# Kernel tuning notes

Measured on AMD Instinct MI355X. Metric: run time of the kernel, lower is better.

Reference implementation:

```python
import jax, jax.numpy as jnp
import numpy as np

EPS = 1e-06


def setup_inputs() -> dict:
    key = jax.random.key(0)
    kq, kk, kv = jax.random.split(key, 3)
    B, H, T, P = 2, 8, 1024, 64
    Q = jax.random.normal(kq, (B, H, T, P), dtype=jnp.float32)
    K = jax.random.normal(kk, (B, H, T, P), dtype=jnp.float32)
    V = jax.random.normal(kv, (B, H, T, P), dtype=jnp.float32)
    return {"Q": Q, "K": K, "V": V}


def _scan_attention(Q, K, V):
    Q_feat = jnp.exp(Q)                                  # (B,H,T,P)
    K_feat = jnp.exp(K)                                  # (B,H,T,P)
    m0 = jnp.log(K_feat)                                 # (B,H,T,P)
    N0 = jnp.einsum('bhtp,bhtn->bhtpn', V, K_feat)       # (B,H,T,P,P) matrix state
    D0 = K_feat                                          # (B,H,T,P)

    def combine(x, y):
        m_x, N_x, D_x = x
        m_y, N_y, D_y = y
        m_new = jnp.maximum(m_x, m_y)
        scale_x = jnp.exp(m_x - m_new)
        scale_y = jnp.exp(m_y - m_new)
        N_new = N_x * scale_x[..., None] + N_y * scale_y[..., None]
        D_new = D_x * scale_x + D_y * scale_y
        return (m_new, N_new, D_new)

    m_cum, num_cum, denom_cum = jax.lax.associative_scan(combine, (m0, N0, D0), axis=2)

    Y_num = jnp.einsum('bhtp,bhtpq->bhtq', Q_feat, num_cum)   # (B,H,T,P)
    Y_den = jnp.einsum('bhtp,bhtp->bht', Q_feat, denom_cum)   # (B,H,T)
    Y = Y_num / (Y_den[..., None] + EPS)
    B, H, T, P = Q.shape
    return Y.transpose(0, 2, 1, 3).reshape(B, T, H * P)


def reference(Q, K, V):
    return _scan_attention(Q, K, V)
```

## Files before the change

kernel.cpp:

```cpp
#include <hip/hip_runtime.h>
#include <hip/hip_bf16.h>

#define TDIM 1024
#define PDIM 64
#define BHN  16
#define SCH  8
#define NSC  128

typedef __bf16 bf16_t;
typedef bf16_t bf16x8 __attribute__((ext_vector_type(8)));
typedef float  floatx4 __attribute__((ext_vector_type(4)));

__device__ __forceinline__ floatx4 mfma16(bf16x8 a, bf16x8 b, floatx4 c) {
    return __builtin_amdgcn_mfma_f32_16x16x32_bf16(a, b, c, 0, 0, 0);
}

__global__ __launch_bounds__(64) void stats_kernel(
        const float* __restrict__ K, float2* __restrict__ stats) {
    int bh = blockIdx.x >> 7;
    int c  = blockIdx.x & 127;
    int p  = threadIdx.x;
    const float* Kb = K + (size_t)bh * TDIM * PDIM + (size_t)c * SCH * PDIM + p;
    float k[SCH];
#pragma unroll
    for (int i = 0; i < SCH; ++i) k[i] = Kb[i * PDIM];
    float m = -INFINITY, s = 0.f;
#pragma unroll
    for (int i = 0; i < SCH; ++i) {
        m = fmaxf(m, k[i]);
        float e = __expf(k[i]);
        s += e * e;
    }
    stats[((size_t)(bh << 7) + c) * PDIM + p] = make_float2(m, s);
}

__global__ __launch_bounds__(512) void featattn_kernel(
        const float* __restrict__ Q, const float* __restrict__ K,
        const float* __restrict__ V, const float2* __restrict__ stats,
        float* __restrict__ out) {
    int bh  = blockIdx.x & 15;
    int i   = blockIdx.x >> 4;
    int tid = threadIdx.x;
    int wave = tid >> 6, lane = tid & 63;
    int lq = lane & 15, qd = lane >> 4;
    int sub = wave & 3;
    int par = wave >> 2;
    int b = bh >> 3, h = bh & 7;

    __shared__ bf16_t Wt[64][72];
    __shared__ bf16_t Ut[2][64][72];
    __shared__ bf16_t Kt[2][64][72];
    __shared__ __align__(16) char ctyraw[8 * 16 * 72 * 2];
    __shared__ float denb[64];
    bf16_t (*Ct)[16][72]  = (bf16_t (*)[16][72])ctyraw;
    float  (*Yred)[16][68] = (float (*)[16][68])ctyraw;

    size_t base = (size_t)bh * TDIM * PDIM;
    int trow = tid >> 3;
    int c0   = (tid & 7) << 3;

    const float* Kst = K + base + (size_t)trow * PDIM + c0;
    const float* Vst = V + base + (size_t)trow * PDIM + c0;
    floatx4 pk0a = *(const floatx4*)(Kst);
    floatx4 pk0b = *(const floatx4*)(Kst + 4);
    floatx4 pv0a = *(const floatx4*)(Vst);
    floatx4 pv0b = *(const floatx4*)(Vst + 4);
    floatx4 pk1a = *(const floatx4*)(Kst + 64 * PDIM);
    floatx4 pk1b = *(const floatx4*)(Kst + 64 * PDIM + 4);
    floatx4 pv1a = *(const floatx4*)(Vst + 64 * PDIM);
    floatx4 pv1b = *(const floatx4*)(Vst + 64 * PDIM + 4);

    {
        int gchunk = 8 * i + wave;
        const float2* st2 = stats + (size_t)(bh << 7) * PDIM + lane;
        float m0 = -INFINITY, m1 = -INFINITY, m2 = -INFINITY, m3 = -INFINITY;
        float s0 = 0.f, s1 = 0.f, s2 = 0.f, s3 = 0.f;
        int cc = 0;
        for (; cc + 4 <= gchunk; cc += 4) {
            float2 v0 = st2[(size_t)(cc + 0) * PDIM];
            float2 v1 = st2[(size_t)(cc + 1) * PDIM];
            float2 v2 = st2[(size_t)(cc + 2) * PDIM];
            float2 v3 = st2[(size_t)(cc + 3) * PDIM];
            m0 = fmaxf(m0, v0.x); s0 += v0.y;
            m1 = fmaxf(m1, v1.x); s1 += v1.y;
            m2 = fmaxf(m2, v2.x); s2 += v2.y;
            m3 = fmaxf(m3, v3.x); s3 += v3.y;
        }
        for (; cc < gchunk; ++cc) {
            float2 v = st2[(size_t)cc * PDIM];
            m0 = fmaxf(m0, v.x); s0 += v.y;
        }
        float m = fmaxf(fmaxf(m0, m1), fmaxf(m2, m3));
        float s = (s0 + s1) + (s2 + s3);

        int t0 = i * 64 + wave * 8;
        float kr[8], qr[8];
#pragma unroll
        for (int j = 0; j < 8; ++j) {
            kr[j] = K[base + (size_t)(t0 + j) * PDIM + lane];
            qr[j] = Q[base + (size_t)(t0 + j) * PDIM + lane];
        }
#pragma unroll
        for (int j = 0; j < 8; ++j) {
            m = fmaxf(m, kr[j]);
            float e = __expf(kr[j]);
            s += e * e;
            float wv = __expf(qr[j] - m);
            Wt[wave * 8 + j][lane] = (bf16_t)wv;
            float d = wv * s;
#pragma unroll
            for (int off = 32; off > 0; off >>= 1) d += __shfl_xor(d, off);
            if (lane == 0) denb[wave * 8 + j] = d;
        }
    }
    __syncthreads();

    bf16x8 a0 = *(const bf16x8*)&Wt[sub * 16 + lq][qd * 8];
    bf16x8 a1 = *(const bf16x8*)&Wt[sub * 16 + lq][32 + qd * 8];

    floatx4 acc[4];
#pragma unroll
    for (int j = 0; j < 4; ++j) acc[j] = (floatx4){0.f, 0.f, 0.f, 0.f};

    int niter = (i >> 1) + 1;
    for (int kt2 = 0; kt2 < niter; ++kt2) {
        __syncthreads();
        {
            float kk[8] = {pk0a.x, pk0a.y, pk0a.z, pk0a.w,
                           pk0b.x, pk0b.y, pk0b.z, pk0b.w};
            float vv[8] = {pv0a.x, pv0a.y, pv0a.z, pv0a.w,
                           pv0b.x, pv0b.y, pv0b.z, pv0b.w};
            bf16x8 uv, kv;
#pragma unroll
            for (int j = 0; j < 8; ++j) {
                float e = __expf(kk[j]);
                kv[j] = (bf16_t)e;
                uv[j] = (bf16_t)(vv[j] * e);
            }
            *(bf16x8*)&Ut[0][trow][c0] = uv;
#pragma unroll
            for (int j = 0; j < 8; ++j) Kt[0][c0 + j][trow] = kv[j];
        }
        {
            float kk[8] = {pk1a.x, pk1a.y, pk1a.z, pk1a.w,
                           pk1b.x, pk1b.y, pk1b.z, pk1b.w};
            float vv[8] = {pv1a.x, pv1a.y, pv1a.z, pv1a.w,
                           pv1b.x, pv1b.y, pv1b.z, pv1b.w};
            bf16x8 uv, kv;
#pragma unroll
            for (int j = 0; j < 8; ++j) {
                float e = __expf(kk[j]);
                kv[j] = (bf16_t)e;
                uv[j] = (bf16_t)(vv[j] * e);
            }
            *(bf16x8*)&Ut[1][trow][c0] = uv;
#pragma unroll
            for (int j = 0; j < 8; ++j) Kt[1][c0 + j][trow] = kv[j];
        }
        if (kt2 + 1 < niter) {
            const float* Kn = Kst + (size_t)(2 * kt2 + 2) * 64 * PDIM;
            const float* Vn = Vst + (size_t)(2 * kt2 + 2) * 64 * PDIM;
            pk0a = *(const floatx4*)(Kn);
            pk0b = *(const floatx4*)(Kn + 4);
            pv0a = *(const floatx4*)(Vn);
            pv0b = *(const floatx4*)(Vn + 4);
            pk1a = *(const floatx4*)(Kn + 64 * PDIM);
            pk1b = *(const floatx4*)(Kn + 64 * PDIM + 4);
            pv1a = *(const floatx4*)(Vn + 64 * PDIM);
            pv1b = *(const floatx4*)(Vn + 64 * PDIM + 4);
        }
        __syncthreads();

        int kt = 2 * kt2 + par;
        if (kt <= i) {
            floatx4 cc4[4];
#pragma unroll
            for (int j = 0; j < 4; ++j) {
                bf16x8 b0 = *(const bf16x8*)&Ut[par][j * 16 + lq][qd * 8];
                bf16x8 b1 = *(const bf16x8*)&Ut[par][j * 16 + lq][32 + qd * 8];
                floatx4 t = (floatx4){0.f, 0.f, 0.f, 0.f};
                t = mfma16(a0, b0, t);
                t = mfma16(a1, b1, t);
                cc4[j] = t;
            }
            int trow0 = i * 64 + sub * 16;
#pragma unroll
            for (int j = 0; j < 4; ++j) {
#pragma unroll
                for (int r = 0; r < 4; ++r) {
                    float v = cc4[j][r];
                    if (kt == i && (kt * 64 + j * 16 + lq) > (trow0 + qd * 4 + r))
                        v = 0.f;
                    Ct[wave][qd * 4 + r][j * 16 + lq] = (bf16_t)v;
                }
            }
            bf16x8 ca0 = *(const bf16x8*)&Ct[wave][lq][qd * 8];
            bf16x8 ca1 = *(const bf16x8*)&Ct[wave][lq][32 + qd * 8];
#pragma unroll
            for (int j = 0; j < 4; ++j) {
                bf16x8 kb0 = *(const bf16x8*)&Kt[par][j * 16 + lq][qd * 8];
                bf16x8 kb1 = *(const bf16x8*)&Kt[par][j * 16 + lq][32 + qd * 8];
                acc[j] = mfma16(ca0, kb0, acc[j]);
                acc[j] = mfma16(ca1, kb1, acc[j]);
            }
        }
    }

    __syncthreads();
    if (par == 1) {
#pragma unroll
        for (int j = 0; j < 4; ++j)
#pragma unroll
            for (int r = 0; r < 4; ++r)
                Yred[sub][qd * 4 + r][j * 16 + lq] = acc[j][r];
    }
    __syncthreads();
    if (par == 0) {
#pragma unroll
        for (int j = 0; j < 4; ++j) {
#pragma unroll
            for (int r = 0; r < 4; ++r) {
                int trow_l = sub * 16 + qd * 4 + r;
                int tg = i * 64 + trow_l;
                float y = acc[j][r] + Yred[sub][qd * 4 + r][j * 16 + lq];
                y = y / (denb[trow_l] + 1e-6f);
                out[((size_t)b * TDIM + tg) * (8 * PDIM) + h * PDIM + j * 16 + lq] = y;
            }
        }
    }
}

extern "C" void kernel_launch(void* const* d_in, const int* in_sizes, int n_in,
                              void* d_out, int out_size, void* d_ws, size_t ws_size,
                              hipStream_t stream) {
    const float* Q = (const float*)d_in[0];
    const float* K = (const float*)d_in[1];
    const float* V = (const float*)d_in[2];
    float* out = (float*)d_out;

    float2* stats = (float2*)d_ws;

    stats_kernel<<<BHN * NSC, 64, 0, stream>>>(K, stats);
    featattn_kernel<<<256, 512, 0, stream>>>(Q, K, V, stats, out);
}
```

Measured before the change: 95.64 us.

## Precompute bf16 exp(K)·V and transposed exp(K) in prep kernel

The stats kernel becomes a prep kernel that also computes U = V·exp(K) and a transposed exp(K) in bf16 and writes both to workspace. The attention kernel then loads these bf16 tiles straight into shared memory with vector stores. This removes the repeated exp work and the strided transposed LDS stores from every block's inner loop, and halves the bytes each block reads. The denominator shuffle reduction is also batched across 8 rows. The cost is an extra global write and read pass, plus more work in the prep kernel.

```diff
diff --git a/kernel.cpp b/kernel.cpp
--- a/kernel.cpp
+++ b/kernel.cpp
@@ -15,29 +15,49 @@
     return __builtin_amdgcn_mfma_f32_16x16x32_bf16(a, b, c, 0, 0, 0);
 }
 
-__global__ __launch_bounds__(64) void stats_kernel(
-        const float* __restrict__ K, float2* __restrict__ stats) {
-    int bh = blockIdx.x >> 7;
-    int c  = blockIdx.x & 127;
+__global__ __launch_bounds__(64) void prep_kernel(
+        const float* __restrict__ K, const float* __restrict__ V,
+        bf16_t* __restrict__ U, bf16_t* __restrict__ Kft,
+        float2* __restrict__ stats) {
+    int bh = blockIdx.x >> 6;
+    int c  = blockIdx.x & 63;
     int p  = threadIdx.x;
-    const float* Kb = K + (size_t)bh * TDIM * PDIM + (size_t)c * SCH * PDIM + p;
-    float k[SCH];
-#pragma unroll
-    for (int i = 0; i < SCH; ++i) k[i] = Kb[i * PDIM];
-    float m = -INFINITY, s = 0.f;
-#pragma unroll
-    for (int i = 0; i < SCH; ++i) {
-        m = fmaxf(m, k[i]);
-        float e = __expf(k[i]);
-        s += e * e;
-    }
-    stats[((size_t)(bh << 7) + c) * PDIM + p] = make_float2(m, s);
+    size_t base = (size_t)bh * TDIM * PDIM;
+    int t0 = c * 16;
+
+    float kq[16], vv[16];
+#pragma unroll
+    for (int i = 0; i < 16; ++i) {
+        kq[i] = K[base + (size_t)(t0 + i) * PDIM + p];
+        vv[i] = V[base + (size_t)(t0 + i) * PDIM + p];
+    }
+
+    __shared__ bf16_t ek_t[16][PDIM + 4];
+    float m0 = -INFINITY, s0 = 0.f, m1 = -INFINITY, s1 = 0.f;
+#pragma unroll
+    for (int i = 0; i < 16; ++i) {
+        float e = __expf(kq[i]);
+        if (i < 8) { m0 = fmaxf(m0, kq[i]); s0 += e * e; }
+        else       { m1 = fmaxf(m1, kq[i]); s1 += e * e; }
+        U[base + (size_t)(t0 + i) * PDIM + p] = (bf16_t)(vv[i] * e);
+        ek_t[i][p] = (bf16_t)e;
+    }
+    stats[((size_t)(bh << 7) + 2 * c + 0) * PDIM + p] = make_float2(m0, s0);
+    stats[((size_t)(bh << 7) + 2 * c + 1) * PDIM + p] = make_float2(m1, s1);
+    __syncthreads();
+
+    int hi = p >> 4, tl = p & 15;
+#pragma unroll
+    for (int it = 0; it < 16; ++it) {
+        int q = it * 4 + hi;
+        Kft[((size_t)bh * PDIM + q) * TDIM + t0 + tl] = ek_t[tl][q];
+    }
 }
 
 __global__ __launch_bounds__(512) void featattn_kernel(
         const float* __restrict__ Q, const float* __restrict__ K,
-        const float* __restrict__ V, const float2* __restrict__ stats,
-        float* __restrict__ out) {
+        const bf16_t* __restrict__ U, const bf16_t* __restrict__ Kft,
+        const float2* __restrict__ stats, float* __restrict__ out) {
     int bh  = blockIdx.x & 15;
     int i   = blockIdx.x >> 4;
     int tid = threadIdx.x;
@@ -56,19 +76,13 @@
     float  (*Yred)[16][68] = (float (*)[16][68])ctyraw;
 
     size_t base = (size_t)bh * TDIM * PDIM;
-    int trow = tid >> 3;
-    int c0   = (tid & 7) << 3;
-
-    const float* Kst = K + base + (size_t)trow * PDIM + c0;
-    const float* Vst = V + base + (size_t)trow * PDIM + c0;
-    floatx4 pk0a = *(const floatx4*)(Kst);
-    floatx4 pk0b = *(const floatx4*)(Kst + 4);
-    floatx4 pv0a = *(const floatx4*)(Vst);
-    floatx4 pv0b = *(const floatx4*)(Vst + 4);
-    floatx4 pk1a = *(const floatx4*)(Kst + 64 * PDIM);
-    floatx4 pk1b = *(const floatx4*)(Kst + 64 * PDIM + 4);
-    floatx4 pv1a = *(const floatx4*)(Vst + 64 * PDIM);
-    floatx4 pv1b = *(const floatx4*)(Vst + 64 * PDIM + 4);
+    size_t kftb = (size_t)bh * PDIM * TDIM;
+    int row = tid >> 3, c8 = (tid & 7) << 3;
+
+    int4 pu0 = *(const int4*)(U + base + (size_t)(0 * 64 + row) * PDIM + c8);
+    int4 pk0 = *(const int4*)(Kft + kftb + (size_t)row * TDIM + 0 * 64 + c8);
+    int4 pu1 = *(const int4*)(U + base + (size_t)(1 * 64 + row) * PDIM + c8);
+    int4 pk1 = *(const int4*)(Kft + kftb + (size_t)row * TDIM + 1 * 64 + c8);
 
     {
         int gchunk = 8 * i + wave;
@@ -94,7 +108,7 @@
         float s = (s0 + s1) + (s2 + s3);
 
         int t0 = i * 64 + wave * 8;
-        float kr[8], qr[8];
+        float kr[8], qr[8], d[8];
 #pragma unroll
         for (int j = 0; j < 8; ++j) {
             kr[j] = K[base + (size_t)(t0 + j) * PDIM + lane];
@@ -107,10 +121,15 @@
             s += e * e;
             float wv = __expf(qr[j] - m);
             Wt[wave * 8 + j][lane] = (bf16_t)wv;
-            float d = wv * s;
-#pragma unroll
-            for (int off = 32; off > 0; off >>= 1) d += __shfl_xor(d, off);
-            if (lane == 0) denb[wave * 8 + j] = d;
+            d[j] = wv * s;
+        }
+#pragma unroll
+        for (int off = 32; off > 0; off >>= 1)
+#pragma unroll
+            for (int j = 0; j < 8; ++j) d[j] += __shfl_xor(d[j], off);
+        if (lane == 0) {
+#pragma unroll
+            for (int j = 0; j < 8; ++j) denb[wave * 8 + j] = d[j];
         }
     }
     __syncthreads();
@@ -125,49 +144,17 @@
     int niter = (i >> 1) + 1;
     for (int kt2 = 0; kt2 < niter; ++kt2) {
         __syncthreads();
-        {
-            float kk[8] = {pk0a.x, pk0a.y, pk0a.z, pk0a.w,
-                           pk0b.x, pk0b.y, pk0b.z, pk0b.w};
-            float vv[8] = {pv0a.x, pv0a.y, pv0a.z, pv0a.w,
-                           pv0b.x, pv0b.y, pv0b.z, pv0b.w};
-            bf16x8 uv, kv;
-#pragma unroll
-            for (int j = 0; j < 8; ++j) {
-                float e = __expf(kk[j]);
-                kv[j] = (bf16_t)e;
-                uv[j] = (bf16_t)(vv[j] * e);
-            }
-            *(bf16x8*)&Ut[0][trow][c0] = uv;
-#pragma unroll
-            for (int j = 0; j < 8; ++j) Kt[0][c0 + j][trow] = kv[j];
-        }
-        {
-            float kk[8] = {pk1a.x, pk1a.y, pk1a.z, pk1a.w,
-                           pk1b.x, pk1b.y, pk1b.z, pk1b.w};
-            float vv[8] = {pv1a.x, pv1a.y, pv1a.z, pv1a.w,
-                           pv1b.x, pv1b.y, pv1b.z, pv1b.w};
-            bf16x8 uv, kv;
-#pragma unroll
-            for (int j = 0; j < 8; ++j) {
-                float e = __expf(kk[j]);
-                kv[j] = (bf16_t)e;
-                uv[j] = (bf16_t)(vv[j] * e);
-            }
-            *(bf16x8*)&Ut[1][trow][c0] = uv;
-#pragma unroll
-            for (int j = 0; j < 8; ++j) Kt[1][c0 + j][trow] = kv[j];
-        }
+        *(int4*)&Ut[0][row][c8] = pu0;
+        *(int4*)&Kt[0][row][c8] = pk0;
+        *(int4*)&Ut[1][row][c8] = pu1;
+        *(int4*)&Kt[1][row][c8] = pk1;
         if (kt2 + 1 < niter) {
-            const float* Kn = Kst + (size_t)(2 * kt2 + 2) * 64 * PDIM;
-            const float* Vn = Vst + (size_t)(2 * kt2 + 2) * 64 * PDIM;
-            pk0a = *(const floatx4*)(Kn);
-            pk0b = *(const floatx4*)(Kn + 4);
-            pv0a = *(const floatx4*)(Vn);
-            pv0b = *(const floatx4*)(Vn + 4);
-            pk1a = *(const floatx4*)(Kn + 64 * PDIM);
-            pk1b = *(const floatx4*)(Kn + 64 * PDIM + 4);
-            pv1a = *(const floatx4*)(Vn + 64 * PDIM);
-            pv1b = *(const floatx4*)(Vn + 64 * PDIM + 4);
+            int ktn = 2 * kt2 + 2;
+            int ktn1 = ktn + 1 > 15 ? 15 : ktn + 1;
+            pu0 = *(const int4*)(U + base + (size_t)(ktn * 64 + row) * PDIM + c8);
+            pk0 = *(const int4*)(Kft + kftb + (size_t)row * TDIM + ktn * 64 + c8);
+            pu1 = *(const int4*)(U + base + (size_t)(ktn1 * 64 + row) * PDIM + c8);
+            pk1 = *(const int4*)(Kft + kftb + (size_t)row * TDIM + ktn1 * 64 + c8);
         }
         __syncthreads();
 
@@ -238,8 +225,10 @@
     const float* V = (const float*)d_in[2];
     float* out = (float*)d_out;
 
-    float2* stats = (float2*)d_ws;
-
-    stats_kernel<<<BHN * NSC, 64, 0, stream>>>(K, stats);
-    featattn_kernel<<<256, 512, 0, stream>>>(Q, K, V, stats, out);
-}
+    bf16_t* Uf   = (bf16_t*)d_ws;
+    bf16_t* Kft  = Uf + (size_t)BHN * TDIM * PDIM;
+    float2* stats = (float2*)(Kft + (size_t)BHN * TDIM * PDIM);
+
+    prep_kernel<<<BHN * 64, 64, 0, stream>>>(K, V, Uf, Kft, stats);
+    featattn_kernel<<<256, 512, 0, stream>>>(Q, K, Uf, Kft, stats, out);
+}
```

New measurement: 88.35 us. -7.6%, faster.
